# Performance work log

Measured on AMD Instinct MI355X. Metric: run time of the kernel, lower is better.

## Reference

```python
import jax, jax.numpy as jnp
import numpy as np

CENTER_LR = 0.5  # EMA learning rate for centers (init arg lr)


def setup_inputs() -> dict:
    key = jax.random.key(0)
    k1, k2, k3 = jax.random.split(key, 3)
    B, D, C = 131072, 256, 1000
    feats = jax.random.normal(k1, (B, D), dtype=jnp.float32)
    centers = jax.random.normal(k2, (C, D), dtype=jnp.float32)
    labels = jax.random.randint(k3, (B,), 0, C, dtype=jnp.int64)
    return {"feats": feats, "centers": centers, "labels": labels}


def reference(feats, centers, labels):
    # EMA center update (done under no_grad in the original):
    # for each class c present in the batch:
    #   centers[c] = (1-lr)*centers[c] + lr*mean(feats[labels==c])
    C = centers.shape[0]
    counts = jax.ops.segment_sum(jnp.ones(labels.shape, feats.dtype), labels,
                                 num_segments=C)                       # [C]
    sums = jax.ops.segment_sum(feats, labels, num_segments=C)          # [C, D]
    means = sums / jnp.maximum(counts, 1.0)[:, None]                   # [C, D]
    present = (counts > 0)[:, None]
    new_centers = jnp.where(present,
                            (1.0 - CENTER_LR) * centers + CENTER_LR * means,
                            centers)                                   # [C, D]
    new_centers = jax.lax.stop_gradient(new_centers)
    # loss = 0.5 * mean_i ||f_i - c_{y_i}||^2
    sel = new_centers[labels]                                          # [B, D]
    diff = feats - sel
    loss = 0.5 * jnp.mean(jnp.sum(diff * diff, axis=1))
    return loss
```

## Files before the change

### kernel.cpp

```cpp
#include <hip/hip_runtime.h>


#define DDIM 256
#define DDIM4 64


__global__ __launch_bounds__(1024) void k0_zero(int* __restrict__ counts,
                                                int* __restrict__ scal16) {
    int t = threadIdx.x;
    counts[t] = 0;
    if (t < 16) scal16[t] = 0;
}

__global__ __launch_bounds__(256) void k1_hist(const int* __restrict__ labels,
                                               int* __restrict__ counts,
                                               int B, int C) {
    __shared__ int h[1024];
    for (int i = threadIdx.x; i < 1024; i += 256) h[i] = 0;
    __syncthreads();
    int stride = gridDim.x * 256;
    for (int i = blockIdx.x * 256 + threadIdx.x; i < B; i += stride)
        atomicAdd(&h[labels[i]], 1);
    __syncthreads();
    for (int i = threadIdx.x; i < C; i += 256) {
        int v = h[i];
        if (v) atomicAdd(&counts[i], v);
    }
}

__global__ __launch_bounds__(1024) void k2_scan(const int* __restrict__ counts,
                                                int* __restrict__ offsets,
                                                int* __restrict__ cursor, int C) {
    __shared__ int sc[1024];
    int t = threadIdx.x;
    int mine = (t < C) ? counts[t] : 0;
    sc[t] = mine;
    __syncthreads();
    for (int off = 1; off < 1024; off <<= 1) {
        int add = (t >= off) ? sc[t - off] : 0;
        __syncthreads();
        sc[t] += add;
        __syncthreads();
    }
    if (t < C) {
        int e = sc[t] - mine;
        offsets[t] = e;
        cursor[t]  = e;
    }
}

__global__ __launch_bounds__(256) void k3_scatter(const int* __restrict__ labels,
                                                  int* __restrict__ cursor,
                                                  int* __restrict__ rowidx, int B) {
    int stride = gridDim.x * 256;
    for (int i = blockIdx.x * 256 + threadIdx.x; i < B; i += stride) {
        int c = labels[i];
        int pos = atomicAdd(&cursor[c], 1);
        rowidx[pos] = i;
    }
}

__global__ __launch_bounds__(256) void k4_class(const float4* __restrict__ feats4,
                                                const float* __restrict__ centers,
                                                const int* __restrict__ rowidx,
                                                const int* __restrict__ counts,
                                                const int* __restrict__ offsets,
                                                float* __restrict__ scalars,
                                                int* __restrict__ ticket,
                                                float* __restrict__ out,
                                                int nblocks, float invB) {
    __shared__ float comb[4 * DDIM];
    __shared__ float red[12];
    __shared__ int lastflag;

    int c = blockIdx.x;
    int count = counts[c];
    int start = offsets[c];
    int t = threadIdx.x, wave = t >> 6, lane = t & 63;

    int per = (count + 3) >> 2;
    int wbeg = wave * per;
    int wend = min(count, wbeg + per);

    float4 acc = make_float4(0.f, 0.f, 0.f, 0.f);
    float ff = 0.f;

    int i = wbeg;
    for (; i + 8 <= wend; i += 8) {
        int j[8];
        float4 v[8];
#pragma unroll
        for (int k = 0; k < 8; ++k) j[k] = rowidx[start + i + k];
#pragma unroll
        for (int k = 0; k < 8; ++k) v[k] = feats4[j[k] * DDIM4 + lane];
#pragma unroll
        for (int k = 0; k < 8; ++k) {
            acc.x += v[k].x; acc.y += v[k].y; acc.z += v[k].z; acc.w += v[k].w;
            ff += v[k].x*v[k].x + v[k].y*v[k].y + v[k].z*v[k].z + v[k].w*v[k].w;
        }
    }
    for (; i < wend; ++i) {
        float4 v = feats4[rowidx[start + i] * DDIM4 + lane];
        acc.x += v.x; acc.y += v.y; acc.z += v.z; acc.w += v.w;
        ff += v.x*v.x + v.y*v.y + v.z*v.z + v.w*v.w;
    }

    comb[wave * DDIM + lane * 4 + 0] = acc.x;
    comb[wave * DDIM + lane * 4 + 1] = acc.y;
    comb[wave * DDIM + lane * 4 + 2] = acc.z;
    comb[wave * DDIM + lane * 4 + 3] = acc.w;
    __syncthreads();

    float s  = comb[t] + comb[DDIM + t] + comb[2 * DDIM + t] + comb[3 * DDIM + t];
    float co = centers[c * DDIM + t];
    float nc = (count > 0) ? 0.5f * co + 0.5f * s / (float)count : co;
    float dotv = nc * s;
    float ccv  = nc * nc * (float)count;

#pragma unroll
    for (int off = 32; off > 0; off >>= 1) {
        ff   += __shfl_down(ff, off);
        dotv += __shfl_down(dotv, off);
        ccv  += __shfl_down(ccv, off);
    }
    if (lane == 0) {
        red[wave * 3 + 0] = ff;
        red[wave * 3 + 1] = dotv;
        red[wave * 3 + 2] = ccv;
    }
    __syncthreads();
    if (t == 0) {
        atomicAdd(&scalars[0], red[0] + red[3] + red[6] + red[9]);
        atomicAdd(&scalars[1], red[1] + red[4] + red[7] + red[10]);
        atomicAdd(&scalars[2], red[2] + red[5] + red[8] + red[11]);
        __threadfence();
        int old = atomicAdd(ticket, 1);
        lastflag = (old == nblocks - 1) ? 1 : 0;
    }
    __syncthreads();
    if (lastflag && t == 0) {
        __threadfence();
        float a = atomicAdd(&scalars[0], 0.f);
        float b = atomicAdd(&scalars[1], 0.f);
        float e = atomicAdd(&scalars[2], 0.f);
        out[0] = 0.5f * invB * (a - 2.f * b + e);
    }
}

extern "C" void kernel_launch(void* const* d_in, const int* in_sizes, int n_in,
                              void* d_out, int out_size, void* d_ws, size_t ws_size,
                              hipStream_t stream) {
    const float* feats   = (const float*)d_in[0];
    const float* centers = (const float*)d_in[1];
    const int*   labels  = (const int*)d_in[2];

    int B = in_sizes[2];
    int Dv = in_sizes[0] / B;
    int C = in_sizes[1] / Dv;
    (void)Dv; (void)n_in; (void)ws_size; (void)out_size;

    int* W = (int*)d_ws;
    int* counts    = W;
    int* offsets   = W + 1024;
    int* cursor    = W + 2048;
    float* scalars = (float*)(W + 3072);
    int* ticket    = W + 3072 + 12;
    int* rowidx    = W + 3072 + 16;

    k0_zero<<<1, 1024, 0, stream>>>(counts, W + 3072);
    k1_hist<<<256, 256, 0, stream>>>(labels, counts, B, C);
    k2_scan<<<1, 1024, 0, stream>>>(counts, offsets, cursor, C);
    int sblocks = (B + 255) / 256;
    if (sblocks > 512) sblocks = 512;
    k3_scatter<<<sblocks, 256, 0, stream>>>(labels, cursor, rowidx, B);
    k4_class<<<C, 256, 0, stream>>>((const float4*)feats, centers, rowidx,
                                    counts, offsets, scalars, ticket,
                                    (float*)d_out, C, 1.0f / (float)B);
}
```

Measured before the change: 116.8 us.

## Replace global sort-and-gather with block-local bucketing, bf16 payload, and LDS reduction

Replaces the global histogram/scan/scatter plus per-class random gather with a per-block bucket sort by label group. It writes feats as a bf16 payload in grouped order while accumulating the squared norms. A second kernel reduces each group of 32 classes into shared-memory tables with LDS atomics, and a small epilogue combines the partials and computes the loss. The aim is to replace random row gathers with streaming accesses. In exchange it adds bf16 rounding of the feature sums and extra intermediate traffic.

```diff
diff --git a/kernel.cpp b/kernel.cpp
--- a/kernel.cpp
+++ b/kernel.cpp
@@ -2,148 +2,216 @@
 
 
 #define DDIM 256
-#define DDIM4 64
-
-
-__global__ __launch_bounds__(1024) void k0_zero(int* __restrict__ counts,
-                                                int* __restrict__ scal16) {
-    int t = threadIdx.x;
-    counts[t] = 0;
-    if (t < 16) scal16[t] = 0;
-}
-
-__global__ __launch_bounds__(256) void k1_hist(const int* __restrict__ labels,
-                                               int* __restrict__ counts,
-                                               int B, int C) {
-    __shared__ int h[1024];
-    for (int i = threadIdx.x; i < 1024; i += 256) h[i] = 0;
-    __syncthreads();
-    int stride = gridDim.x * 256;
-    for (int i = blockIdx.x * 256 + threadIdx.x; i < B; i += stride)
-        atomicAdd(&h[labels[i]], 1);
-    __syncthreads();
-    for (int i = threadIdx.x; i < C; i += 256) {
-        int v = h[i];
-        if (v) atomicAdd(&counts[i], v);
-    }
-}
-
-__global__ __launch_bounds__(1024) void k2_scan(const int* __restrict__ counts,
-                                                int* __restrict__ offsets,
-                                                int* __restrict__ cursor, int C) {
-    __shared__ int sc[1024];
-    int t = threadIdx.x;
-    int mine = (t < C) ? counts[t] : 0;
-    sc[t] = mine;
-    __syncthreads();
-    for (int off = 1; off < 1024; off <<= 1) {
-        int add = (t >= off) ? sc[t - off] : 0;
-        __syncthreads();
-        sc[t] += add;
-        __syncthreads();
-    }
-    if (t < C) {
-        int e = sc[t] - mine;
-        offsets[t] = e;
-        cursor[t]  = e;
-    }
-}
-
-__global__ __launch_bounds__(256) void k3_scatter(const int* __restrict__ labels,
-                                                  int* __restrict__ cursor,
-                                                  int* __restrict__ rowidx, int B) {
-    int stride = gridDim.x * 256;
-    for (int i = blockIdx.x * 256 + threadIdx.x; i < B; i += stride) {
-        int c = labels[i];
-        int pos = atomicAdd(&cursor[c], 1);
-        rowidx[pos] = i;
-    }
-}
-
-__global__ __launch_bounds__(256) void k4_class(const float4* __restrict__ feats4,
-                                                const float* __restrict__ centers,
-                                                const int* __restrict__ rowidx,
-                                                const int* __restrict__ counts,
-                                                const int* __restrict__ offsets,
-                                                float* __restrict__ scalars,
-                                                int* __restrict__ ticket,
-                                                float* __restrict__ out,
-                                                int nblocks, float invB) {
-    __shared__ float comb[4 * DDIM];
-    __shared__ float red[12];
-    __shared__ int lastflag;
-
-    int c = blockIdx.x;
-    int count = counts[c];
-    int start = offsets[c];
+#define ROWS_PB 256
+#define NGRP 16
+
+__device__ __forceinline__ unsigned short f2bf(float x) {
+    unsigned u = __float_as_uint(x);
+    unsigned r = (u + 0x7FFFu + ((u >> 16) & 1u)) >> 16;
+    return (unsigned short)r;
+}
+__device__ __forceinline__ float bf2f(unsigned short b) {
+    return __uint_as_float(((unsigned)b) << 16);
+}
+
+__global__ __launch_bounds__(64) void k0_zero(float* __restrict__ scal16) {
+    if (threadIdx.x < 16) scal16[threadIdx.x] = 0.f;
+}
+
+__global__ __launch_bounds__(512) void kA_sort(const float* __restrict__ feats,
+                                               const int* __restrict__ labels,
+                                               ushort4* __restrict__ pay,
+                                               unsigned char* __restrict__ glab,
+                                               int* __restrict__ mat,
+                                               float* __restrict__ scalars) {
+    __shared__ ushort4 payL[ROWS_PB * 64];
+    __shared__ int map[ROWS_PB];
+    __shared__ unsigned char locL[ROWS_PB];
+    __shared__ int h[32], cur[32], scan[33];
+    __shared__ float redf[8];
+
+    int b = blockIdx.x, t = threadIdx.x, wave = t >> 6, lane = t & 63;
+    int gbase = b * ROWS_PB;
+
+    if (t < 32) h[t] = 0;
+    __syncthreads();
+    int mylbl = 0;
+    if (t < ROWS_PB) {
+        mylbl = labels[gbase + t];
+        atomicAdd(&h[mylbl >> 5], 1);
+    }
+    __syncthreads();
+    if (t == 0) {
+        int s = 0;
+#pragma unroll
+        for (int i = 0; i < 32; ++i) { scan[i] = s; s += h[i]; }
+        scan[32] = s;
+    }
+    __syncthreads();
+    if (t < 32) cur[t] = scan[t];
+    if (t < 33) mat[b * 33 + t] = scan[t];
+    __syncthreads();
+    if (t < ROWS_PB) {
+        int pos = atomicAdd(&cur[mylbl >> 5], 1);
+        map[t] = pos;
+        locL[pos] = (unsigned char)(mylbl & 31);
+    }
+    __syncthreads();
+
+    float ff = 0.f;
+    int r0 = wave * 32;
+    for (int it = 0; it < 4; ++it) {
+        int rb = r0 + it * 8;
+        float v[8][4];
+#pragma unroll
+        for (int j = 0; j < 8; ++j) {
+            const float* rp = feats + (size_t)(gbase + rb + j) * DDIM + lane;
+            v[j][0] = rp[0];
+            v[j][1] = rp[64];
+            v[j][2] = rp[128];
+            v[j][3] = rp[192];
+        }
+#pragma unroll
+        for (int j = 0; j < 8; ++j) {
+            ff += v[j][0]*v[j][0] + v[j][1]*v[j][1]
+                + v[j][2]*v[j][2] + v[j][3]*v[j][3];
+            ushort4 o;
+            o.x = f2bf(v[j][0]); o.y = f2bf(v[j][1]);
+            o.z = f2bf(v[j][2]); o.w = f2bf(v[j][3]);
+            int srow = map[rb + j];
+            payL[srow * 64 + lane] = o;
+        }
+    }
+    __syncthreads();
+
+    {
+        ushort4* dst = pay + (size_t)gbase * 64;
+        for (int idx = t; idx < ROWS_PB * 64; idx += 512) dst[idx] = payL[idx];
+        if (t < ROWS_PB) glab[gbase + t] = locL[t];
+    }
+
+#pragma unroll
+    for (int off = 32; off > 0; off >>= 1) ff += __shfl_xor(ff, off);
+    if (lane == 0) redf[wave] = ff;
+    __syncthreads();
+    if (t == 0) {
+        float a = 0.f;
+#pragma unroll
+        for (int w = 0; w < 8; ++w) a += redf[w];
+        atomicAdd(&scalars[0], a);
+    }
+}
+
+__global__ __launch_bounds__(512) void kB_reduce(const ushort4* __restrict__ pay,
+                                                 const unsigned char* __restrict__ glab,
+                                                 const int* __restrict__ mat,
+                                                 float* __restrict__ part,
+                                                 int* __restrict__ counts_part,
+                                                 int nA) {
+    __shared__ float table[32 * DDIM];
+    __shared__ int m0L[32], m1L[32], ccnt[32];
+
+    int bid = blockIdx.x;
+    int q = bid >> 4, g = bid & (NGRP - 1);
     int t = threadIdx.x, wave = t >> 6, lane = t & 63;
-
-    int per = (count + 3) >> 2;
-    int wbeg = wave * per;
-    int wend = min(count, wbeg + per);
-
-    float4 acc = make_float4(0.f, 0.f, 0.f, 0.f);
-    float ff = 0.f;
-
-    int i = wbeg;
-    for (; i + 8 <= wend; i += 8) {
-        int j[8];
-        float4 v[8];
-#pragma unroll
-        for (int k = 0; k < 8; ++k) j[k] = rowidx[start + i + k];
-#pragma unroll
-        for (int k = 0; k < 8; ++k) v[k] = feats4[j[k] * DDIM4 + lane];
-#pragma unroll
-        for (int k = 0; k < 8; ++k) {
-            acc.x += v[k].x; acc.y += v[k].y; acc.z += v[k].z; acc.w += v[k].w;
-            ff += v[k].x*v[k].x + v[k].y*v[k].y + v[k].z*v[k].z + v[k].w*v[k].w;
-        }
-    }
-    for (; i < wend; ++i) {
-        float4 v = feats4[rowidx[start + i] * DDIM4 + lane];
-        acc.x += v.x; acc.y += v.y; acc.z += v.z; acc.w += v.w;
-        ff += v.x*v.x + v.y*v.y + v.z*v.z + v.w*v.w;
-    }
-
-    comb[wave * DDIM + lane * 4 + 0] = acc.x;
-    comb[wave * DDIM + lane * 4 + 1] = acc.y;
-    comb[wave * DDIM + lane * 4 + 2] = acc.z;
-    comb[wave * DDIM + lane * 4 + 3] = acc.w;
-    __syncthreads();
-
-    float s  = comb[t] + comb[DDIM + t] + comb[2 * DDIM + t] + comb[3 * DDIM + t];
-    float co = centers[c * DDIM + t];
-    float nc = (count > 0) ? 0.5f * co + 0.5f * s / (float)count : co;
-    float dotv = nc * s;
-    float ccv  = nc * nc * (float)count;
+    int srcpb = nA / NGRP;
+
+    for (int idx = t; idx < 32 * DDIM; idx += 512) table[idx] = 0.f;
+    if (t < 32) {
+        ccnt[t] = 0;
+        int b = g * srcpb + t;
+        m0L[t] = mat[b * 33 + q];
+        m1L[t] = mat[b * 33 + q + 1];
+    }
+    __syncthreads();
+
+    for (int bb = wave * 4; bb < wave * 4 + 4; ++bb) {
+        int m0 = m0L[bb], m1 = m1L[bb];
+        int base = (g * srcpb + bb) * ROWS_PB;
+        int r = m0;
+        for (; r + 4 <= m1; r += 4) {
+            ushort4 u[4];
+            int loc[4];
+#pragma unroll
+            for (int j = 0; j < 4; ++j)
+                u[j] = pay[(size_t)(base + r + j) * 64 + lane];
+#pragma unroll
+            for (int j = 0; j < 4; ++j)
+                loc[j] = glab[base + r + j];
+#pragma unroll
+            for (int j = 0; j < 4; ++j) {
+                float* tb = &table[loc[j] * DDIM + lane];
+                atomicAdd(tb,       bf2f(u[j].x));
+                atomicAdd(tb + 64,  bf2f(u[j].y));
+                atomicAdd(tb + 128, bf2f(u[j].z));
+                atomicAdd(tb + 192, bf2f(u[j].w));
+                if (lane == 0) atomicAdd(&ccnt[loc[j]], 1);
+            }
+        }
+        for (; r < m1; ++r) {
+            ushort4 u = pay[(size_t)(base + r) * 64 + lane];
+            int loc = glab[base + r];
+            float* tb = &table[loc * DDIM + lane];
+            atomicAdd(tb,       bf2f(u.x));
+            atomicAdd(tb + 64,  bf2f(u.y));
+            atomicAdd(tb + 128, bf2f(u.z));
+            atomicAdd(tb + 192, bf2f(u.w));
+            if (lane == 0) atomicAdd(&ccnt[loc], 1);
+        }
+    }
+    __syncthreads();
+
+    {
+        const float4* t4 = (const float4*)table;
+        float4* p4 = (float4*)&part[((size_t)g * 1024 + q * 32) * DDIM];
+        for (int idx = t; idx < 32 * DDIM / 4; idx += 512) p4[idx] = t4[idx];
+        if (t < 32) counts_part[g * 1024 + q * 32 + t] = ccnt[t];
+    }
+}
+
+__global__ __launch_bounds__(64) void k_epi(const float* __restrict__ part,
+                                            const int* __restrict__ counts_part,
+                                            const float* __restrict__ centers,
+                                            float* __restrict__ scalars,
+                                            int* __restrict__ ticket,
+                                            float* __restrict__ out,
+                                            int C, float invB) {
+    int c = blockIdx.x, lane = threadIdx.x;
+    float4 s = make_float4(0.f, 0.f, 0.f, 0.f);
+    int n = 0;
+#pragma unroll
+    for (int g = 0; g < NGRP; ++g) {
+        float4 p = *(const float4*)&part[((size_t)g * 1024 + c) * DDIM + lane * 4];
+        s.x += p.x; s.y += p.y; s.z += p.z; s.w += p.w;
+        n += counts_part[g * 1024 + c];
+    }
+    float4 co = *(const float4*)&centers[c * DDIM + lane * 4];
+    float inv = (n > 0) ? 0.5f / (float)n : 0.f;
+    float4 nc;
+    nc.x = 0.5f * co.x + s.x * inv;
+    nc.y = 0.5f * co.y + s.y * inv;
+    nc.z = 0.5f * co.z + s.z * inv;
+    nc.w = 0.5f * co.w + s.w * inv;
+    float dotv = nc.x * s.x + nc.y * s.y + nc.z * s.z + nc.w * s.w;
+    float ccv  = (nc.x*nc.x + nc.y*nc.y + nc.z*nc.z + nc.w*nc.w) * (float)n;
 
 #pragma unroll
     for (int off = 32; off > 0; off >>= 1) {
-        ff   += __shfl_down(ff, off);
         dotv += __shfl_down(dotv, off);
         ccv  += __shfl_down(ccv, off);
     }
     if (lane == 0) {
-        red[wave * 3 + 0] = ff;
-        red[wave * 3 + 1] = dotv;
-        red[wave * 3 + 2] = ccv;
-    }
-    __syncthreads();
-    if (t == 0) {
-        atomicAdd(&scalars[0], red[0] + red[3] + red[6] + red[9]);
-        atomicAdd(&scalars[1], red[1] + red[4] + red[7] + red[10]);
-        atomicAdd(&scalars[2], red[2] + red[5] + red[8] + red[11]);
+        atomicAdd(&scalars[1], dotv);
+        atomicAdd(&scalars[2], ccv);
         __threadfence();
         int old = atomicAdd(ticket, 1);
-        lastflag = (old == nblocks - 1) ? 1 : 0;
-    }
-    __syncthreads();
-    if (lastflag && t == 0) {
-        __threadfence();
-        float a = atomicAdd(&scalars[0], 0.f);
-        float b = atomicAdd(&scalars[1], 0.f);
-        float e = atomicAdd(&scalars[2], 0.f);
-        out[0] = 0.5f * invB * (a - 2.f * b + e);
+        if (old == C - 1) {
+            __threadfence();
+            float A  = atomicAdd(&scalars[0], 0.f);
+            float Bv = atomicAdd(&scalars[1], 0.f);
+            float E  = atomicAdd(&scalars[2], 0.f);
+            out[0] = 0.5f * invB * (A - 2.f * Bv + E);
+        }
     }
 }
 
@@ -159,21 +227,25 @@
     int C = in_sizes[1] / Dv;
     (void)Dv; (void)n_in; (void)ws_size; (void)out_size;
 
+    int nA = B / ROWS_PB;
+
     int* W = (int*)d_ws;
-    int* counts    = W;
-    int* offsets   = W + 1024;
-    int* cursor    = W + 2048;
-    float* scalars = (float*)(W + 3072);
-    int* ticket    = W + 3072 + 12;
-    int* rowidx    = W + 3072 + 16;
-
-    k0_zero<<<1, 1024, 0, stream>>>(counts, W + 3072);
-    k1_hist<<<256, 256, 0, stream>>>(labels, counts, B, C);
-    k2_scan<<<1, 1024, 0, stream>>>(counts, offsets, cursor, C);
-    int sblocks = (B + 255) / 256;
-    if (sblocks > 512) sblocks = 512;
-    k3_scatter<<<sblocks, 256, 0, stream>>>(labels, cursor, rowidx, B);
-    k4_class<<<C, 256, 0, stream>>>((const float4*)feats, centers, rowidx,
-                                    counts, offsets, scalars, ticket,
-                                    (float*)d_out, C, 1.0f / (float)B);
-}
+    float* scalars   = (float*)W;
+    int* ticket      = W + 12;
+    int* mat         = W + 16;
+    int* counts_part = mat + nA * 33;
+    unsigned char* glab = (unsigned char*)(counts_part + NGRP * 1024);
+    int lab_ints = B / 4;
+    int* after_lab = counts_part + NGRP * 1024 + lab_ints;
+    size_t off = (size_t)(after_lab - W);
+    off = (off + 3) & ~(size_t)3;
+    float* part = (float*)(W + off);
+    ushort4* pay = (ushort4*)(part + (size_t)NGRP * 1024 * DDIM);
+
+    k0_zero<<<1, 64, 0, stream>>>(scalars);
+    kA_sort<<<nA, 512, 0, stream>>>(feats, labels, pay, glab, mat, scalars);
+    kB_reduce<<<32 * NGRP, 512, 0, stream>>>(pay, glab, mat, part,
+                                             counts_part, nA);
+    k_epi<<<C, 64, 0, stream>>>(part, counts_part, centers, scalars, ticket,
+                                (float*)d_out, C, 1.0f / (float)B);
+}
```

After: 277.8 us. 2.38x slower.
